# Performance work log

Measured on AMD Instinct MI355X. Metric: run time of the kernel, lower is better.

Reference implementation:

```python
import jax, jax.numpy as jnp
import numpy as np

B, T, C, H = 4, 2048, 1024, 16
HD = C // H


def setup_inputs() -> dict:
    key = jax.random.key(0)
    k1, k2, k3 = jax.random.split(key, 3)
    x = jax.random.normal(k1, (B, T, C), dtype=jnp.float32)
    w_attn = jax.random.normal(k2, (C, 3 * C), dtype=jnp.float32) * (1.0 / np.sqrt(C))
    b_attn = jnp.zeros((3 * C,), dtype=jnp.float32)
    w_proj = jax.random.normal(k3, (C, C), dtype=jnp.float32) * (1.0 / np.sqrt(C))
    b_proj = jnp.zeros((C,), dtype=jnp.float32)
    return {"x": x, "w_attn": w_attn, "b_attn": b_attn, "w_proj": w_proj, "b_proj": b_proj}


def reference(x, w_attn, b_attn, w_proj, b_proj):
    # QKV projection: [B,T,3C]
    qkv = x @ w_attn + b_attn
    q, k, v = jnp.split(qkv, 3, axis=-1)
    # [B,H,T,HD]
    q = q.reshape(B, T, H, HD).swapaxes(1, 2)
    k = k.reshape(B, T, H, HD).swapaxes(1, 2)
    v = v.reshape(B, T, H, HD).swapaxes(1, 2)
    scale = 1.0 / jnp.sqrt(jnp.float32(HD))
    attn = jnp.einsum('bhqd,bhkd->bhqk', q, k) * scale  # [B,H,T,T]
    causal = jnp.tril(jnp.ones((T, T), dtype=bool))
    attn = jnp.where(causal[None, None, :, :], attn, -jnp.inf)
    attn = jax.nn.softmax(attn, axis=-1)
    y = jnp.einsum('bhqk,bhkd->bhqd', attn, v)  # [B,H,T,HD]
    y = y.swapaxes(1, 2).reshape(B, T, C)
    return y @ w_proj + b_proj
```

## Files before the change

### kernel.cpp

```cpp
#include <hip/hip_runtime.h>
#include <hip/hip_bf16.h>

#define BB 4
#define TT 2048
#define CC 1024
#define HH 16
#define HD 64
#define NQ (3*CC)
#define QSCALE 0.18033688011112042f

typedef __attribute__((ext_vector_type(8))) short bf16x8;
typedef __attribute__((ext_vector_type(4))) short short4_t;
typedef __attribute__((ext_vector_type(4))) float f32x4;

#define MFMA(a,b,c) __builtin_amdgcn_mfma_f32_16x16x32_bf16(a,b,c,0,0,0)

#define ASYNC16(gsrc, ldst) \
  __builtin_amdgcn_global_load_lds((const __attribute__((address_space(1))) void*)(gsrc), \
                                   (__attribute__((address_space(3))) void*)(ldst), 16, 0, 0)

#define SWZA(row) (((((row) & 7) + (((row) >> 3) & 3)) & 7) << 3)

static __device__ __forceinline__ short f2bf(float f){
    union { float f; unsigned u; } v; v.f = f;
    unsigned r = v.u + 0x7FFFu + ((v.u >> 16) & 1u);
    return (short)(r >> 16);
}
static __device__ __forceinline__ short f2bfu(float f){
    union { float f; unsigned u; } v; v.f = f;
    return (short)((v.u + 0x8000u) >> 16);
}

__global__ __launch_bounds__(256)
void convert_x(const float* __restrict__ x, short* __restrict__ xb)
{
    int i = (blockIdx.x * 256 + threadIdx.x) * 8;
    float4 a = *reinterpret_cast<const float4*>(&x[i]);
    float4 b = *reinterpret_cast<const float4*>(&x[i+4]);
    bf16x8 o = { f2bf(a.x), f2bf(a.y), f2bf(a.z), f2bf(a.w),
                 f2bf(b.x), f2bf(b.y), f2bf(b.z), f2bf(b.w) };
    *reinterpret_cast<bf16x8*>(&xb[i]) = o;
}

__global__ __launch_bounds__(256)
void transpose_w(const float* __restrict__ w, short* __restrict__ wT, int N)
{
    __shared__ short sm[64*72];
    const int kt0 = blockIdx.x * 64;
    const int nt0 = blockIdx.y * 64;
    const int t = threadIdx.x;
    const int r  = t >> 4;
    const int c4 = (t & 15) * 4;
#pragma unroll
    for (int it = 0; it < 4; it++){
        int k = r + it*16;
        float4 v = *reinterpret_cast<const float4*>(&w[(size_t)(kt0 + k)*N + nt0 + c4]);
        sm[(c4+0)*72 + k] = f2bf(v.x);
        sm[(c4+1)*72 + k] = f2bf(v.y);
        sm[(c4+2)*72 + k] = f2bf(v.z);
        sm[(c4+3)*72 + k] = f2bf(v.w);
    }
    __syncthreads();
    const int nl = t >> 2;
    const int kc = (t & 3) * 16;
    bf16x8 o0 = *reinterpret_cast<const bf16x8*>(&sm[nl*72 + kc]);
    bf16x8 o1 = *reinterpret_cast<const bf16x8*>(&sm[nl*72 + kc + 8]);
    short* dst = &wT[(size_t)(nt0 + nl)*CC + kt0 + kc];
    *reinterpret_cast<bf16x8*>(dst)     = o0;
    *reinterpret_cast<bf16x8*>(dst + 8) = o1;
}

__global__ __launch_bounds__(256, 2)
void qkv_gemm(const short* __restrict__ xb, const short* __restrict__ wT,
              const float* __restrict__ bias,
              short* __restrict__ qb, short* __restrict__ kb, short* __restrict__ vb)
{
    __shared__ short As[128*64];
    __shared__ short Bs[128*64];
    const int bid = blockIdx.x;
    const int swz = (bid & 7) * 192 + (bid >> 3);
    const int bm = swz / (NQ/128);
    const int bn = swz % (NQ/128);
    const int m0 = bm*128, n0 = bn*128;
    const int t  = threadIdx.x;
    const int wid = t >> 6, lane = t & 63;
    const int wr = wid >> 1, wc = wid & 1;
    const int l15 = lane & 15, lh = lane >> 4;

    f32x4 acc[4][4];
#pragma unroll
    for (int i=0;i<4;i++)
#pragma unroll
      for (int j=0;j<4;j++) acc[i][j] = (f32x4)0.f;

    for (int k0 = 0; k0 < CC; k0 += 64) {
        __syncthreads();
#pragma unroll
        for (int i=0;i<4;i++){
            int u   = (wid*4 + i)*64 + lane;
            int row = u >> 3, c = u & 7;
            int cs  = c ^ (row & 7);
            ASYNC16(&xb[(size_t)(m0+row)*CC + k0 + cs*8], &As[(wid*4+i)*512]);
            ASYNC16(&wT[(size_t)(n0+row)*CC + k0 + cs*8], &Bs[(wid*4+i)*512]);
        }
        __syncthreads();
#pragma unroll
        for (int ks=0;ks<2;ks++){
            bf16x8 a[4], b[4];
#pragma unroll
            for (int m=0;m<4;m++){
                int row = wr*64 + m*16 + l15;
                a[m] = *reinterpret_cast<const bf16x8*>(&As[row*64 + (((ks<<2)|lh) ^ (row&7))*8]);
            }
#pragma unroll
            for (int n=0;n<4;n++){
                int col = wc*64 + n*16 + l15;
                b[n] = *reinterpret_cast<const bf16x8*>(&Bs[col*64 + (((ks<<2)|lh) ^ (col&7))*8]);
            }
#pragma unroll
            for (int m=0;m<4;m++)
#pragma unroll
              for (int n=0;n<4;n++)
                acc[m][n] = MFMA(a[m], b[n], acc[m][n]);
        }
    }

#pragma unroll
    for (int n=0;n<4;n++){
        int col = n0 + wc*64 + n*16 + l15;
        int sect = col >> 10;
        int cc = col & 1023;
        int h = cc >> 6, d = cc & 63;
        float bv = bias[col];
        short* dst = (sect==0) ? qb : (sect==1) ? kb : vb;
        float mul = (sect==0) ? QSCALE : 1.f;
#pragma unroll
        for (int m=0;m<4;m++)
#pragma unroll
          for (int r=0;r<4;r++){
            int row = m0 + wr*64 + m*16 + lh*4 + r;
            int b_ = row >> 11, tt_ = row & (TT-1);
            float v = (acc[m][n][r] + bv) * mul;
            dst[((size_t)(b_*HH + h)*TT + tt_)*HD + d] = f2bf(v);
          }
    }
}

__global__ __launch_bounds__(256, 2)
void attn_kernel(const short* __restrict__ qb, const short* __restrict__ kb,
                 const short* __restrict__ vb, short* __restrict__ yb)
{
    __shared__ short Ks[2][64*64];
    __shared__ short Vt[2][64*64];
    __shared__ short Ps[4][32*64];

    const int bh = blockIdx.x;
    const int p  = blockIdx.y;
    const int b_ = bh >> 4, h = bh & 15;
    const short* qp = qb + (size_t)bh*TT*HD;
    const short* kp = kb + (size_t)bh*TT*HD;
    const short* vp = vb + (size_t)bh*TT*HD;
    const int t = threadIdx.x, wid = t >> 6, lane = t & 63;
    const int l15 = lane & 15, lh = lane >> 4;
    const int vd4  = (t & 15) * 4;
    const int vkv4 = (t >> 4) * 4;
    const int krow = t >> 3;
    const int kdq  = (t & 7) * 8;

    const bf16x8 ones = { 0x3F80,0x3F80,0x3F80,0x3F80,0x3F80,0x3F80,0x3F80,0x3F80 };

    for (int hf = 0; hf < 2; hf++){
        const int qt  = hf ? (15 - p) : p;
        const int wq0 = qt*128 + wid*32;

        bf16x8 qf[2][2];
#pragma unroll
        for (int m=0;m<2;m++)
#pragma unroll
          for (int ks=0;ks<2;ks++)
            qf[m][ks] = *reinterpret_cast<const bf16x8*>(
                &qp[(size_t)(wq0 + m*16 + l15)*HD + ks*32 + lh*8]);

        f32x4 po[2][4];
        f32x4 pden[2];
#pragma unroll
        for (int m=0;m<2;m++){
            pden[m] = (f32x4)0.f;
#pragma unroll
            for (int n=0;n<4;n++) po[m][n] = (f32x4)0.f;
        }

        const int ntk = 2*(qt + 1);

        {
            bf16x8 ka = *reinterpret_cast<const bf16x8*>(&kp[(size_t)(krow)*HD + kdq]);
            bf16x8 kc = *reinterpret_cast<const bf16x8*>(&kp[(size_t)(32+krow)*HD + kdq]);
            short4_t r0 = *reinterpret_cast<const short4_t*>(&vp[(size_t)(vkv4+0)*HD + vd4]);
            short4_t r1 = *reinterpret_cast<const short4_t*>(&vp[(size_t)(vkv4+1)*HD + vd4]);
            short4_t r2 = *reinterpret_cast<const short4_t*>(&vp[(size_t)(vkv4+2)*HD + vd4]);
            short4_t r3 = *reinterpret_cast<const short4_t*>(&vp[(size_t)(vkv4+3)*HD + vd4]);
            *reinterpret_cast<bf16x8*>(&Ks[0][(krow*64 + kdq) ^ SWZA(krow)]) = ka;
            *reinterpret_cast<bf16x8*>(&Ks[0][((32+krow)*64 + kdq) ^ SWZA(32+krow)]) = kc;
#pragma unroll
            for (int c=0;c<4;c++){
                short4_t pk = { r0[c], r1[c], r2[c], r3[c] };
                int dd = vd4 + c;
                *reinterpret_cast<short4_t*>(&Vt[0][(dd*64 + vkv4) ^ SWZA(dd)]) = pk;
            }
        }
        __syncthreads();

        for (int kt = 0; kt < ntk; kt++){
            const int cur = kt & 1;
            const int kv0 = kt*64;
            const bool pf = (kt+1 < ntk);
            bf16x8 ka, kc; short4_t r0, r1, r2, r3;
            if (pf){
                const int kn = kv0 + 64;
                ka = *reinterpret_cast<const bf16x8*>(&kp[(size_t)(kn+krow)*HD + kdq]);
                kc = *reinterpret_cast<const bf16x8*>(&kp[(size_t)(kn+32+krow)*HD + kdq]);
                r0 = *reinterpret_cast<const short4_t*>(&vp[(size_t)(kn+vkv4+0)*HD + vd4]);
                r1 = *reinterpret_cast<const short4_t*>(&vp[(size_t)(kn+vkv4+1)*HD + vd4]);
                r2 = *reinterpret_cast<const short4_t*>(&vp[(size_t)(kn+vkv4+2)*HD + vd4]);
                r3 = *reinterpret_cast<const short4_t*>(&vp[(size_t)(kn+vkv4+3)*HD + vd4]);
            }

            if (kv0 <= wq0 + 31){
                f32x4 s[2][4];
#pragma unroll
                for (int m=0;m<2;m++)
#pragma unroll
                  for (int f=0;f<4;f++) s[m][f] = (f32x4)0.f;
                __builtin_amdgcn_s_setprio(1);
#pragma unroll
                for (int ks=0;ks<2;ks++){
#pragma unroll
                    for (int f=0;f<4;f++){
                        int kvr = f*16 + l15;
                        bf16x8 kf = *reinterpret_cast<const bf16x8*>(
                            &Ks[cur][(kvr*64 + ks*32 + lh*8) ^ SWZA(kvr)]);
                        s[0][f] = MFMA(kf, qf[0][ks], s[0][f]);
                        s[1][f] = MFMA(kf, qf[1][ks], s[1][f]);
                    }
                }
                __builtin_amdgcn_s_setprio(0);
#pragma unroll
                for (int m=0;m<2;m++){
                    if (kv0 + 63 > wq0 + m*16){
                        int qm = wq0 + m*16 + l15;
#pragma unroll
                        for (int f=0;f<4;f++)
#pragma unroll
                          for (int r=0;r<4;r++){
                            int kv = kv0 + f*16 + lh*4 + r;
                            if (kv > qm) s[m][f][r] = -1e30f;
                          }
                    }
                }
#pragma unroll
                for (int m=0;m<2;m++){
                    int qloc = m*16 + l15;
                    int rowswz = SWZA(qloc);
#pragma unroll
                    for (int f=0;f<4;f++){
                        short4_t pk = { f2bfu(exp2f(s[m][f][0])),
                                        f2bfu(exp2f(s[m][f][1])),
                                        f2bfu(exp2f(s[m][f][2])),
                                        f2bfu(exp2f(s[m][f][3])) };
                        int idx = (qloc*64 + f*16 + lh*4) ^ rowswz;
                        *reinterpret_cast<short4_t*>(&Ps[wid][idx]) = pk;
                    }
                }
                __builtin_amdgcn_s_setprio(1);
#pragma unroll
                for (int ks2=0;ks2<2;ks2++){
                    bf16x8 pa[2];
#pragma unroll
                    for (int m=0;m<2;m++){
                        int qloc = m*16 + l15;
                        pa[m] = *reinterpret_cast<const bf16x8*>(
                            &Ps[wid][(qloc*64 + ks2*32 + lh*8) ^ SWZA(qloc)]);
                    }
                    pden[0] = MFMA(pa[0], ones, pden[0]);
                    pden[1] = MFMA(pa[1], ones, pden[1]);
#pragma unroll
                    for (int n=0;n<4;n++){
                        int dd = n*16 + l15;
                        bf16x8 vf = *reinterpret_cast<const bf16x8*>(
                            &Vt[cur][(dd*64 + ks2*32 + lh*8) ^ SWZA(dd)]);
                        po[0][n] = MFMA(pa[0], vf, po[0][n]);
                        po[1][n] = MFMA(pa[1], vf, po[1][n]);
                    }
                }
                __builtin_amdgcn_s_setprio(0);
            }

            if (pf){
                const int nxt = cur ^ 1;
                *reinterpret_cast<bf16x8*>(&Ks[nxt][(krow*64 + kdq) ^ SWZA(krow)]) = ka;
                *reinterpret_cast<bf16x8*>(&Ks[nxt][((32+krow)*64 + kdq) ^ SWZA(32+krow)]) = kc;
#pragma unroll
                for (int c=0;c<4;c++){
                    short4_t pk = { r0[c], r1[c], r2[c], r3[c] };
                    int dd = vd4 + c;
                    *reinterpret_cast<short4_t*>(&Vt[nxt][(dd*64 + vkv4) ^ SWZA(dd)]) = pk;
                }
                __syncthreads();
            }
        }

#pragma unroll
        for (int m=0;m<2;m++){
            float rcp[4];
#pragma unroll
            for (int r=0;r<4;r++) rcp[r] = 1.f / pden[m][r];
#pragma unroll
            for (int n=0;n<4;n++)
#pragma unroll
              for (int r=0;r<4;r++){
                int q = wq0 + m*16 + lh*4 + r;
                int dd = n*16 + l15;
                yb[(size_t)(b_*TT + q)*CC + h*HD + dd] = f2bf(po[m][n][r] * rcp[r]);
              }
        }
    }
}

__global__ __launch_bounds__(256, 2)
void proj_gemm(const short* __restrict__ y, const short* __restrict__ wpT,
               const float* __restrict__ bias, float* __restrict__ out)
{
    __shared__ short As[128*64];
    __shared__ short Bs[128*64];
    const int bid = blockIdx.x;
    const int swz = (bid & 7) * 64 + (bid >> 3);
    const int bm = swz >> 3, bn = swz & 7;
    const int m0 = bm*128, n0 = bn*128;
    const int t  = threadIdx.x;
    const int wid = t >> 6, lane = t & 63;
    const int wr = wid >> 1, wc = wid & 1;
    const int l15 = lane & 15, lh = lane >> 4;

    f32x4 acc[4][4];
#pragma unroll
    for (int i=0;i<4;i++)
#pragma unroll
      for (int j=0;j<4;j++) acc[i][j] = (f32x4)0.f;

    for (int k0 = 0; k0 < CC; k0 += 64) {
        __syncthreads();
#pragma unroll
        for (int i=0;i<4;i++){
            int u   = (wid*4 + i)*64 + lane;
            int row = u >> 3, c = u & 7;
            int cs  = c ^ (row & 7);
            ASYNC16(&y[(size_t)(m0+row)*CC + k0 + cs*8],   &As[(wid*4+i)*512]);
            ASYNC16(&wpT[(size_t)(n0+row)*CC + k0 + cs*8], &Bs[(wid*4+i)*512]);
        }
        __syncthreads();
#pragma unroll
        for (int ks=0;ks<2;ks++){
            bf16x8 a[4], b[4];
#pragma unroll
            for (int m=0;m<4;m++){
                int row = wr*64 + m*16 + l15;
                a[m] = *reinterpret_cast<const bf16x8*>(&As[row*64 + (((ks<<2)|lh) ^ (row&7))*8]);
            }
#pragma unroll
            for (int n=0;n<4;n++){
                int col = wc*64 + n*16 + l15;
                b[n] = *reinterpret_cast<const bf16x8*>(&Bs[col*64 + (((ks<<2)|lh) ^ (col&7))*8]);
            }
#pragma unroll
            for (int m=0;m<4;m++)
#pragma unroll
              for (int n=0;n<4;n++)
                acc[m][n] = MFMA(a[m], b[n], acc[m][n]);
        }
    }

#pragma unroll
    for (int n=0;n<4;n++){
        int col = n0 + wc*64 + n*16 + l15;
        float bv = bias[col];
#pragma unroll
        for (int m=0;m<4;m++)
#pragma unroll
          for (int r=0;r<4;r++){
            int row = m0 + wr*64 + m*16 + lh*4 + r;
            out[(size_t)row*CC + col] = acc[m][n][r] + bv;
          }
    }
}

extern "C" void kernel_launch(void* const* d_in, const int* in_sizes, int n_in,
                              void* d_out, int out_size, void* d_ws, size_t ws_size,
                              hipStream_t stream) {
    const float* x      = (const float*)d_in[0];
    const float* w_attn = (const float*)d_in[1];
    const float* b_attn = (const float*)d_in[2];
    const float* w_proj = (const float*)d_in[3];
    const float* b_proj = (const float*)d_in[4];
    float* out = (float*)d_out;

    const size_t S = (size_t)BB*TT*CC;
    short* qb  = (short*)d_ws;
    short* kb  = qb + S;
    short* vb  = kb + S;
    short* yx  = vb + S;
    short* wT  = yx + S;
    short* wpT = wT + (size_t)NQ*CC;

    convert_x<<<dim3(S/(256*8)), 256, 0, stream>>>(x, yx);
    transpose_w<<<dim3(CC/64, NQ/64), 256, 0, stream>>>(w_attn, wT, NQ);
    transpose_w<<<dim3(CC/64, CC/64), 256, 0, stream>>>(w_proj, wpT, CC);
    qkv_gemm<<<dim3((BB*TT/128)*(NQ/128)), 256, 0, stream>>>(yx, wT, b_attn, qb, kb, vb);
    attn_kernel<<<dim3(BB*HH, TT/256), 256, 0, stream>>>(qb, kb, vb, yx);
    proj_gemm<<<dim3((BB*TT/128)*(CC/128)), 256, 0, stream>>>(yx, wpT, b_proj, out);
}
```

Before: 187.8 us.

## Pre-transpose V and stage K/V tiles with async global-to-LDS loads

Adds a separate kernel that transposes V into a [bh, d, t] buffer, so the attention kernel can fill its K and transposed-V shared tiles with direct global_load_lds copies instead of register loads followed by scalar transposing LDS writes. The swizzle is applied through the source address, so each lane's 16-byte chunk lands in the swizzled slot. The launch bound rises to three blocks per CU. In exchange there is an extra kernel launch plus a full extra pass over V, and a barrier now runs on every iteration.

```diff
diff --git a/kernel.cpp b/kernel.cpp
--- a/kernel.cpp
+++ b/kernel.cpp
@@ -66,6 +66,31 @@
     bf16x8 o0 = *reinterpret_cast<const bf16x8*>(&sm[nl*72 + kc]);
     bf16x8 o1 = *reinterpret_cast<const bf16x8*>(&sm[nl*72 + kc + 8]);
     short* dst = &wT[(size_t)(nt0 + nl)*CC + kt0 + kc];
+    *reinterpret_cast<bf16x8*>(dst)     = o0;
+    *reinterpret_cast<bf16x8*>(dst + 8) = o1;
+}
+
+__global__ __launch_bounds__(256)
+void transpose_v(const short* __restrict__ vb, short* __restrict__ vtb)
+{
+    __shared__ short sm[64*72];
+    const int bh = blockIdx.x;
+    const int t0 = blockIdx.y * 64;
+    const int t = threadIdx.x;
+    const int r   = t >> 2;
+    const int c16 = (t & 3) * 16;
+    const short* src = vb + (size_t)bh*TT*HD + (size_t)t0*HD;
+    bf16x8 a0 = *reinterpret_cast<const bf16x8*>(&src[r*HD + c16]);
+    bf16x8 a1 = *reinterpret_cast<const bf16x8*>(&src[r*HD + c16 + 8]);
+#pragma unroll
+    for (int j=0;j<8;j++){
+        sm[(c16+j)*72 + r]   = a0[j];
+        sm[(c16+8+j)*72 + r] = a1[j];
+    }
+    __syncthreads();
+    bf16x8 o0 = *reinterpret_cast<const bf16x8*>(&sm[r*72 + c16]);
+    bf16x8 o1 = *reinterpret_cast<const bf16x8*>(&sm[r*72 + c16 + 8]);
+    short* dst = vtb + (size_t)bh*HD*TT + (size_t)r*TT + t0 + c16;
     *reinterpret_cast<bf16x8*>(dst)     = o0;
     *reinterpret_cast<bf16x8*>(dst + 8) = o1;
 }
@@ -146,9 +171,9 @@
     }
 }
 
-__global__ __launch_bounds__(256, 2)
+__global__ __launch_bounds__(256, 3)
 void attn_kernel(const short* __restrict__ qb, const short* __restrict__ kb,
-                 const short* __restrict__ vb, short* __restrict__ yb)
+                 const short* __restrict__ vtb, short* __restrict__ yb)
 {
     __shared__ short Ks[2][64*64];
     __shared__ short Vt[2][64*64];
@@ -157,17 +182,25 @@
     const int bh = blockIdx.x;
     const int p  = blockIdx.y;
     const int b_ = bh >> 4, h = bh & 15;
-    const short* qp = qb + (size_t)bh*TT*HD;
-    const short* kp = kb + (size_t)bh*TT*HD;
-    const short* vp = vb + (size_t)bh*TT*HD;
+    const short* qp  = qb  + (size_t)bh*TT*HD;
+    const short* kp  = kb  + (size_t)bh*TT*HD;
+    const short* vtp = vtb + (size_t)bh*HD*TT;
     const int t = threadIdx.x, wid = t >> 6, lane = t & 63;
     const int l15 = lane & 15, lh = lane >> 4;
-    const int vd4  = (t & 15) * 4;
-    const int vkv4 = (t >> 4) * 4;
-    const int krow = t >> 3;
-    const int kdq  = (t & 7) * 8;
+
+    const int su0 = (wid*2+0)*64 + lane;
+    const int su1 = (wid*2+1)*64 + lane;
+    const int sr0 = su0 >> 3, sc0 = (su0 & 7) ^ (SWZA(su0 >> 3) >> 3);
+    const int sr1 = su1 >> 3, sc1 = (su1 & 7) ^ (SWZA(su1 >> 3) >> 3);
 
     const bf16x8 ones = { 0x3F80,0x3F80,0x3F80,0x3F80,0x3F80,0x3F80,0x3F80,0x3F80 };
+
+    auto stage = [&](int buf, int kvbase){
+        ASYNC16(&kp[(size_t)(kvbase+sr0)*HD + sc0*8], &Ks[buf][(wid*2+0)*512]);
+        ASYNC16(&kp[(size_t)(kvbase+sr1)*HD + sc1*8], &Ks[buf][(wid*2+1)*512]);
+        ASYNC16(&vtp[(size_t)sr0*TT + kvbase + sc0*8], &Vt[buf][(wid*2+0)*512]);
+        ASYNC16(&vtp[(size_t)sr1*TT + kvbase + sc1*8], &Vt[buf][(wid*2+1)*512]);
+    };
 
     for (int hf = 0; hf < 2; hf++){
         const int qt  = hf ? (15 - p) : p;
@@ -192,38 +225,13 @@
 
         const int ntk = 2*(qt + 1);
 
-        {
-            bf16x8 ka = *reinterpret_cast<const bf16x8*>(&kp[(size_t)(krow)*HD + kdq]);
-            bf16x8 kc = *reinterpret_cast<const bf16x8*>(&kp[(size_t)(32+krow)*HD + kdq]);
-            short4_t r0 = *reinterpret_cast<const short4_t*>(&vp[(size_t)(vkv4+0)*HD + vd4]);
-            short4_t r1 = *reinterpret_cast<const short4_t*>(&vp[(size_t)(vkv4+1)*HD + vd4]);
-            short4_t r2 = *reinterpret_cast<const short4_t*>(&vp[(size_t)(vkv4+2)*HD + vd4]);
-            short4_t r3 = *reinterpret_cast<const short4_t*>(&vp[(size_t)(vkv4+3)*HD + vd4]);
-            *reinterpret_cast<bf16x8*>(&Ks[0][(krow*64 + kdq) ^ SWZA(krow)]) = ka;
-            *reinterpret_cast<bf16x8*>(&Ks[0][((32+krow)*64 + kdq) ^ SWZA(32+krow)]) = kc;
-#pragma unroll
-            for (int c=0;c<4;c++){
-                short4_t pk = { r0[c], r1[c], r2[c], r3[c] };
-                int dd = vd4 + c;
-                *reinterpret_cast<short4_t*>(&Vt[0][(dd*64 + vkv4) ^ SWZA(dd)]) = pk;
-            }
-        }
+        stage(0, 0);
         __syncthreads();
 
         for (int kt = 0; kt < ntk; kt++){
             const int cur = kt & 1;
             const int kv0 = kt*64;
-            const bool pf = (kt+1 < ntk);
-            bf16x8 ka, kc; short4_t r0, r1, r2, r3;
-            if (pf){
-                const int kn = kv0 + 64;
-                ka = *reinterpret_cast<const bf16x8*>(&kp[(size_t)(kn+krow)*HD + kdq]);
-                kc = *reinterpret_cast<const bf16x8*>(&kp[(size_t)(kn+32+krow)*HD + kdq]);
-                r0 = *reinterpret_cast<const short4_t*>(&vp[(size_t)(kn+vkv4+0)*HD + vd4]);
-                r1 = *reinterpret_cast<const short4_t*>(&vp[(size_t)(kn+vkv4+1)*HD + vd4]);
-                r2 = *reinterpret_cast<const short4_t*>(&vp[(size_t)(kn+vkv4+2)*HD + vd4]);
-                r3 = *reinterpret_cast<const short4_t*>(&vp[(size_t)(kn+vkv4+3)*HD + vd4]);
-            }
+            if (kt+1 < ntk) stage(cur ^ 1, kv0 + 64);
 
             if (kv0 <= wq0 + 31){
                 f32x4 s[2][4];
@@ -295,18 +303,7 @@
                 __builtin_amdgcn_s_setprio(0);
             }
 
-            if (pf){
-                const int nxt = cur ^ 1;
-                *reinterpret_cast<bf16x8*>(&Ks[nxt][(krow*64 + kdq) ^ SWZA(krow)]) = ka;
-                *reinterpret_cast<bf16x8*>(&Ks[nxt][((32+krow)*64 + kdq) ^ SWZA(32+krow)]) = kc;
-#pragma unroll
-                for (int c=0;c<4;c++){
-                    short4_t pk = { r0[c], r1[c], r2[c], r3[c] };
-                    int dd = vd4 + c;
-                    *reinterpret_cast<short4_t*>(&Vt[nxt][(dd*64 + vkv4) ^ SWZA(dd)]) = pk;
-                }
-                __syncthreads();
-            }
+            __syncthreads();
         }
 
 #pragma unroll
@@ -410,11 +407,13 @@
     short* yx  = vb + S;
     short* wT  = yx + S;
     short* wpT = wT + (size_t)NQ*CC;
+    short* vtb = wpT + (size_t)CC*CC;
 
     convert_x<<<dim3(S/(256*8)), 256, 0, stream>>>(x, yx);
     transpose_w<<<dim3(CC/64, NQ/64), 256, 0, stream>>>(w_attn, wT, NQ);
     transpose_w<<<dim3(CC/64, CC/64), 256, 0, stream>>>(w_proj, wpT, CC);
     qkv_gemm<<<dim3((BB*TT/128)*(NQ/128)), 256, 0, stream>>>(yx, wT, b_attn, qb, kb, vb);
-    attn_kernel<<<dim3(BB*HH, TT/256), 256, 0, stream>>>(qb, kb, vb, yx);
+    transpose_v<<<dim3(BB*HH, TT/64), 256, 0, stream>>>(vb, vtb);
+    attn_kernel<<<dim3(BB*HH, TT/256), 256, 0, stream>>>(qb, kb, vtb, yx);
     proj_gemm<<<dim3((BB*TT/128)*(CC/128)), 256, 0, stream>>>(yx, wpT, b_proj, out);
 }
```

After: 191.6 us. 1.02x slower.
